# Kernel optimization log

Measured on AMD Instinct MI355X. Metric: run time of the kernel, lower is better.

The kernel has to match this reference:

```python
import jax, jax.numpy as jnp
import numpy as np

B, CIN, H, W = 4, 64, 160, 160
G, K = 8, 3
KK = K * K
PAD = K // 2
CG = CIN // G  # channels per deformable group


def setup_inputs() -> dict:
    key = jax.random.key(0)
    ks = jax.random.split(key, 6)
    x = jax.random.normal(ks[0], (B, CIN, H, W), jnp.float32)
    feat = jax.random.normal(ks[1], (B, CIN, H, W), jnp.float32)
    # conv_offset weights (zero-init in the original; small random here so offsets are nontrivial)
    w_off = jax.random.normal(ks[2], (3 * G * KK, CIN, 3, 3), jnp.float32) * 0.01
    b_off = jax.random.normal(ks[3], (3 * G * KK,), jnp.float32) * 0.01
    # deformable conv weights (torchvision DeformConv2d: groups=1, bias=True)
    w_dcn = jax.random.normal(ks[4], (CIN, CIN, K, K), jnp.float32) * (1.0 / np.sqrt(CIN * KK))
    b_dcn = jax.random.normal(ks[5], (CIN,), jnp.float32) * 0.01
    return dict(x=x, feat=feat, w_off=w_off, b_off=b_off, w_dcn=w_dcn, b_dcn=b_dcn)


def _modulated_deform_conv(x, offset, mask, w, b):
    # x: [B,C,H,W]; offset: [B,2*G*KK,H,W] (interleaved dy,dx per (g,k));
    # mask: [B,G*KK,H,W]; w: [Cout,C,K,K]; stride 1, zero padding K//2.
    Bn, C, Hh, Ww = x.shape
    off = offset.reshape(Bn, G, KK, 2, Hh, Ww)
    dy = off[:, :, :, 0]  # [B,G,KK,H,W]
    dx = off[:, :, :, 1]
    ki = jnp.arange(K)
    base_y = (jnp.repeat(ki, K) - PAD).reshape(1, 1, KK, 1, 1).astype(x.dtype)
    base_x = (jnp.tile(ki, K) - PAD).reshape(1, 1, KK, 1, 1).astype(x.dtype)
    hy = jnp.arange(Hh, dtype=x.dtype).reshape(1, 1, 1, Hh, 1)
    wx = jnp.arange(Ww, dtype=x.dtype).reshape(1, 1, 1, 1, Ww)
    py = hy + base_y + dy  # sample rows  [B,G,KK,H,W]
    px = wx + base_x + dx  # sample cols
    y0 = jnp.floor(py)
    x0 = jnp.floor(px)
    ly = py - y0
    lx = px - x0
    y0i = y0.astype(jnp.int32)
    x0i = x0.astype(jnp.int32)
    xg = x.reshape(Bn, G, CG, Hh * Ww)

    def gather(yi, xi):
        valid = ((yi >= 0) & (yi < Hh) & (xi >= 0) & (xi < Ww)).astype(x.dtype)
        idx = jnp.clip(yi, 0, Hh - 1) * Ww + jnp.clip(xi, 0, Ww - 1)
        flat = idx.reshape(Bn, G, 1, KK * Hh * Ww)
        v = jnp.take_along_axis(xg, flat, axis=3).reshape(Bn, G, CG, KK, Hh, Ww)
        return v * valid[:, :, None]  # zero padding outside

    v = ((1 - ly) * (1 - lx))[:, :, None] * gather(y0i, x0i) \
      + ((1 - ly) * lx)[:, :, None] * gather(y0i, x0i + 1) \
      + (ly * (1 - lx))[:, :, None] * gather(y0i + 1, x0i) \
      + (ly * lx)[:, :, None] * gather(y0i + 1, x0i + 1)
    v = v * mask.reshape(Bn, G, 1, KK, Hh, Ww)
    wr = w.reshape(w.shape[0], G, CG, KK)
    out = jnp.einsum('ogck,bgckhw->bohw', wr, v) + b[None, :, None, None]
    return out


def reference(x, feat, w_off, b_off, w_dcn, b_dcn):
    # conv_offset: 3x3 conv, stride 1, pad 1
    out = jax.lax.conv_general_dilated(
        feat, w_off, (1, 1), ((1, 1), (1, 1)),
        dimension_numbers=('NCHW', 'OIHW', 'NCHW')) + b_off[None, :, None, None]
    o1, o2, m = jnp.split(out, 3, axis=1)
    offset = jnp.concatenate([o1, o2], axis=1)  # [B, 2*G*KK, H, W]
    mask = jax.nn.sigmoid(m)                    # [B, G*KK, H, W]
    return _modulated_deform_conv(x, offset, mask, w_dcn, b_dcn)
```

## Files before the change

kernel.cpp:

```cpp
#include <hip/hip_runtime.h>
#include <math.h>

#define Bn   4
#define CINc 64
#define Hh   160
#define Ww   160
#define Gg   8
#define HW   (Hh * Ww)
#define COFF 216

#define OROW 220
#define VROW 200
#define OFFS_SZ (64 * OROW)
#define UNION_SZ 12800

typedef short bf16x8 __attribute__((ext_vector_type(8)));
typedef float f32x4  __attribute__((ext_vector_type(4)));

static __device__ __forceinline__ unsigned short f2bf(float f) {
    unsigned int u = __float_as_uint(f);
    u = (u + 0x7fffu + ((u >> 16) & 1u)) >> 16;
    return (unsigned short)u;
}
static __device__ __forceinline__ float bf2f(unsigned short s) {
    return __uint_as_float(((unsigned int)s) << 16);
}
static __device__ __forceinline__ float blo(unsigned int u) {
    return __uint_as_float(u << 16);
}
static __device__ __forceinline__ float bhi(unsigned int u) {
    return __uint_as_float(u & 0xffff0000u);
}

#define WB 180
__global__ __launch_bounds__(256)
void prep_kernel(const float* __restrict__ feat, const float* __restrict__ x,
                 const float* __restrict__ w_off, const float* __restrict__ w_dcn,
                 unsigned short* __restrict__ featT, unsigned short* __restrict__ xG,
                 unsigned short* __restrict__ wofrag, unsigned short* __restrict__ wfrag) {
    const int blk = blockIdx.x;
    const int t = threadIdx.x;
    if (blk < 1280) {
        __shared__ float tile[CINc][161];
        const int isx = blk >= 640;
        const int rem = isx ? blk - 640 : blk;
        const int b = rem / Hh;
        const int h = rem % Hh;
        const float* src = isx ? x : feat;
        for (int i = t; i < CINc * (Ww / 4); i += 256) {
            int ci = i / (Ww / 4), w4 = i % (Ww / 4);
            float4 v = *(const float4*)(src + (((size_t)b * CINc + ci) * Hh + h) * Ww + w4 * 4);
            tile[ci][w4 * 4 + 0] = v.x; tile[ci][w4 * 4 + 1] = v.y;
            tile[ci][w4 * 4 + 2] = v.z; tile[ci][w4 * 4 + 3] = v.w;
        }
        __syncthreads();
        if (isx) {
            for (int i = t; i < CINc * Ww / 2; i += 256) {
                int g = i / (Ww * 4);
                int r = i % (Ww * 4);
                int w = r >> 2, cp = r & 3;
                unsigned int lo = f2bf(tile[g * 8 + 2 * cp][w]);
                unsigned int hi = f2bf(tile[g * 8 + 2 * cp + 1][w]);
                *(unsigned int*)(xG + (((size_t)b * Gg + g) * HW + h * Ww + w) * 8 + 2 * cp)
                    = lo | (hi << 16);
            }
        } else {
            for (int i = t; i < CINc * Ww / 2; i += 256) {
                int w = i / (CINc / 2), cp = i % (CINc / 2);
                unsigned int lo = f2bf(tile[2 * cp][w]);
                unsigned int hi = f2bf(tile[2 * cp + 1][w]);
                *(unsigned int*)(featT + (((size_t)b * Hh + h) * Ww + w) * CINc + 2 * cp)
                    = lo | (hi << 16);
            }
        }
    } else {
        for (int e = (blk - 1280) * 256 + t; e < 147456 + 36864; e += WB * 256) {
            if (e < 147456) {
                const int j    = e & 7;
                const int lane = (e >> 3) & 63;
                const int rest = e >> 9;
                const int mt = rest & 15;
                const int q  = rest >> 4;
                const int ks = q & 1;
                const int kp = q >> 1;
                const int co = mt * 16 + (lane & 15);
                const int ci = ks * 32 + (lane >> 4) * 8 + j;
                float v = (co < COFF) ? w_off[(size_t)co * 576 + ci * 9 + kp] : 0.f;
                wofrag[e] = f2bf(v);
            } else {
                const int e2   = e - 147456;
                const int j    = e2 & 7;
                const int lane = (e2 >> 3) & 63;
                const int mt   = (e2 >> 9) & 3;
                const int ks   = e2 >> 11;
                const int m = mt * 16 + (lane & 15);
                const int k = ks * 32 + (lane >> 4) * 8 + j;
                const int g = k / 72, r = k % 72;
                const int kk = r >> 3, cg = r & 7;
                const int ci = g * 8 + cg;
                wfrag[e2] = f2bf(w_dcn[((size_t)m * CINc + ci) * 9 + kk]);
            }
        }
    }
}

#define BLEND_J(out_, w00, w01, w10, w11, c00, c01, c10, c11) {            \
    float vl_ = (c00) * blo(w00) + (c01) * blo(w01)                        \
              + (c10) * blo(w10) + (c11) * blo(w11);                       \
    float vh_ = (c00) * bhi(w00) + (c01) * bhi(w01)                        \
              + (c10) * bhi(w10) + (c11) * bhi(w11);                       \
    asm("v_cvt_pk_bf16_f32 %0, %1, %2" : "=v"(out_) : "v"(vl_), "v"(vh_)); \
}

__global__ __launch_bounds__(256, 3)
void dcnpack_fused(const unsigned short* __restrict__ featT,
                   const unsigned short* __restrict__ xG,
                   const unsigned short* __restrict__ wofrag,
                   const unsigned short* __restrict__ wfrag,
                   const float* __restrict__ b_off,
                   const float* __restrict__ b_dcn,
                   float* __restrict__ out) {
    __shared__ unsigned short smem[OFFS_SZ + UNION_SZ];
    unsigned short* offs = smem;
    unsigned short* halo = smem + OFFS_SZ;
    unsigned short* vbuf = smem + OFFS_SZ;

    const int b  = blockIdx.z;
    const int h0 = blockIdx.y * 8;
    const int w0 = blockIdx.x * 8;
    const int t  = threadIdx.x;
    const int wv   = t >> 6;
    const int lane = t & 63;
    const int n    = lane & 15;
    const int kg   = lane >> 4;

    for (int task = t; task < 800; task += 256) {
        const int pix = task >> 3, ch = task & 7;
        const int ry = pix / 10, rx = pix % 10;
        const int gh = h0 - 1 + ry, gw = w0 - 1 + rx;
        float4 v = make_float4(0.f, 0.f, 0.f, 0.f);
        if (gh >= 0 && gh < Hh && gw >= 0 && gw < Ww)
            v = *(const float4*)(featT + ((((size_t)b * Hh) + gh) * Ww + gw) * CINc + ch * 8);
        *(float4*)(halo + pix * 72 + ch * 8) = v;
    }
    __syncthreads();

    const int bbase0 = (((n >> 3) * 10) + (n & 7)) * 72 + kg * 8;

    f32x4 cacc[4][4] = {};
    bf16x8 af[3][4];
    #pragma unroll
    for (int i = 0; i < 4; ++i)
        af[0][i] = *(const bf16x8*)(wofrag + (((size_t)0 * 16 + wv + 4 * i) * 64 + lane) * 8);
    #pragma unroll
    for (int i = 0; i < 4; ++i)
        af[1][i] = *(const bf16x8*)(wofrag + (((size_t)1 * 16 + wv + 4 * i) * 64 + lane) * 8);

    #pragma unroll
    for (int s = 0; s < 18; ++s) {
        if (s + 2 < 18) {
            #pragma unroll
            for (int i = 0; i < 4; ++i)
                af[(s + 2) % 3][i] = *(const bf16x8*)(wofrag +
                    (((size_t)(s + 2) * 16 + wv + 4 * i) * 64 + lane) * 8);
        }
        const int kp = s >> 1, ks = s & 1;
        const int ky = kp / 3, kx = kp % 3;
        #pragma unroll
        for (int nt = 0; nt < 4; ++nt) {
            const bf16x8 bfr = *(const bf16x8*)(halo + bbase0 + nt * 1440 +
                                                (ky * 10 + kx) * 72 + ks * 32);
            #pragma unroll
            for (int i = 0; i < 4; ++i)
                cacc[i][nt] = __builtin_amdgcn_mfma_f32_16x16x32_bf16(af[s % 3][i], bfr, cacc[i][nt], 0, 0, 0);
        }
    }

    #pragma unroll
    for (int i = 0; i < 4; ++i) {
        const int mt = wv + 4 * i;
        #pragma unroll
        for (int r = 0; r < 4; ++r) {
            const int co = mt * 16 + kg * 4 + r;
            if (co < COFF) {
                const float bias = b_off[co];
                const int ismask = (co >= 144);
                const int gk = ismask ? (co - 144) : (co >> 1);
                const int type = ismask ? 2 : (co & 1);
                #pragma unroll
                for (int nt = 0; nt < 4; ++nt) {
                    const int p = nt * 16 + n;
                    float v = cacc[i][nt][r] + bias;
                    if (ismask) v = 1.f / (1.f + expf(-v));
                    offs[p * OROW + gk * 3 + type] = f2bf(v);
                }
            }
        }
    }
    __syncthreads();

    f32x4 dacc[4] = {};
    const int p_t = t & 63;
    const int h_s = h0 + (p_t >> 3);
    const int w_s = w0 + (p_t & 7);

    for (int c = 0; c < 3; ++c) {
        float cf[6][4];
        uint4 q[6][4];
        #pragma unroll
        for (int it = 0; it < 6; ++it) {
            const int u = c * 24 + wv + it * 4;
            const int g = u / 9;
            const int k = u % 9;

            const float dy   = bf2f(offs[p_t * OROW + u * 3 + 0]);
            const float dx   = bf2f(offs[p_t * OROW + u * 3 + 1]);
            const float mask = bf2f(offs[p_t * OROW + u * 3 + 2]);

            const float py  = (float)h_s + (float)(k / 3 - 1) + dy;
            const float pxx = (float)w_s + (float)(k % 3 - 1) + dx;
            const float y0f = floorf(py), x0f = floorf(pxx);
            const float ly = py - y0f, lx = pxx - x0f;
            const int y0 = (int)y0f, x0i = (int)x0f;
            const int y1 = y0 + 1,  x1  = x0i + 1;

            const float vy0 = (y0 >= 0 && y0 < Hh) ? 1.f : 0.f;
            const float vy1 = (y1 >= 0 && y1 < Hh) ? 1.f : 0.f;
            const float vx0 = (x0i >= 0 && x0i < Ww) ? 1.f : 0.f;
            const float vx1 = (x1 >= 0 && x1 < Ww) ? 1.f : 0.f;

            cf[it][0] = (1.f - ly) * (1.f - lx) * vy0 * vx0 * mask;
            cf[it][1] = (1.f - ly) * lx         * vy0 * vx1 * mask;
            cf[it][2] = ly         * (1.f - lx) * vy1 * vx0 * mask;
            cf[it][3] = ly         * lx         * vy1 * vx1 * mask;

            const int y0c = min(max(y0, 0), Hh - 1), y1c = min(max(y1, 0), Hh - 1);
            const int x0c = min(max(x0i, 0), Ww - 1), x1c = min(max(x1, 0), Ww - 1);

            const unsigned short* xb = xG + ((size_t)b * Gg + g) * HW * 8;
            q[it][0] = *(const uint4*)(xb + ((size_t)y0c * Ww + x0c) * 8);
            q[it][1] = *(const uint4*)(xb + ((size_t)y0c * Ww + x1c) * 8);
            q[it][2] = *(const uint4*)(xb + ((size_t)y1c * Ww + x0c) * 8);
            q[it][3] = *(const uint4*)(xb + ((size_t)y1c * Ww + x1c) * 8);
        }

        #pragma unroll
        for (int it = 0; it < 6; ++it) {
            unsigned int rr0, rr1, rr2, rr3;
            BLEND_J(rr0, q[it][0].x, q[it][1].x, q[it][2].x, q[it][3].x,
                    cf[it][0], cf[it][1], cf[it][2], cf[it][3]);
            BLEND_J(rr1, q[it][0].y, q[it][1].y, q[it][2].y, q[it][3].y,
                    cf[it][0], cf[it][1], cf[it][2], cf[it][3]);
            BLEND_J(rr2, q[it][0].z, q[it][1].z, q[it][2].z, q[it][3].z,
                    cf[it][0], cf[it][1], cf[it][2], cf[it][3]);
            BLEND_J(rr3, q[it][0].w, q[it][1].w, q[it][2].w, q[it][3].w,
                    cf[it][0], cf[it][1], cf[it][2], cf[it][3]);
            uint4 res; res.x = rr0; res.y = rr1; res.z = rr2; res.w = rr3;
            *(uint4*)(vbuf + (size_t)p_t * VROW + (wv + it * 4) * 8) = res;
        }

        bf16x8 afr[6];
        #pragma unroll
        for (int s = 0; s < 6; ++s)
            afr[s] = *(const bf16x8*)(wfrag + (((size_t)(c * 6 + s) * 4 + wv) * 64 + lane) * 8);

        __syncthreads();

        #pragma unroll
        for (int s = 0; s < 6; ++s) {
            #pragma unroll
            for (int nt = 0; nt < 4; ++nt) {
                const bf16x8 bfr = *(const bf16x8*)(vbuf + (nt * 16 + n) * VROW + s * 32 + kg * 8);
                dacc[nt] = __builtin_amdgcn_mfma_f32_16x16x32_bf16(afr[s], bfr, dacc[nt], 0, 0, 0);
            }
        }
        __syncthreads();
    }

    #pragma unroll
    for (int nt = 0; nt < 4; ++nt) {
        const int p = nt * 16 + n;
        const int h = h0 + (p >> 3);
        const int w = w0 + (p & 7);
        #pragma unroll
        for (int r = 0; r < 4; ++r) {
            const int o = wv * 16 + kg * 4 + r;
            out[(((size_t)b * CINc + o) * HW) + h * Ww + w] = dacc[nt][r] + b_dcn[o];
        }
    }
}

extern "C" void kernel_launch(void* const* d_in, const int* in_sizes, int n_in,
                              void* d_out, int out_size, void* d_ws, size_t ws_size,
                              hipStream_t stream) {
    const float* x     = (const float*)d_in[0];
    const float* feat  = (const float*)d_in[1];
    const float* w_off = (const float*)d_in[2];
    const float* b_off = (const float*)d_in[3];
    const float* w_dcn = (const float*)d_in[4];
    const float* b_dcn = (const float*)d_in[5];
    float* out = (float*)d_out;

    unsigned short* featT  = (unsigned short*)d_ws;
    unsigned short* xG     = featT + (size_t)Bn * HW * CINc;
    unsigned short* wofrag = xG + (size_t)Bn * HW * CINc;
    unsigned short* wfrag  = wofrag + (size_t)147456;

    prep_kernel<<<dim3(1280 + WB), 256, 0, stream>>>(
        feat, x, w_off, w_dcn, featT, xG, wofrag, wfrag);
    dcnpack_fused<<<dim3(Ww / 8, Hh / 8, Bn), 256, 0, stream>>>(
        featT, xG, wofrag, wfrag, b_off, b_dcn, out);
}
```

Baseline: 192.3 us.

## Split fused DCN kernel into offset-conv and sampling-GEMM kernels

Splits the single fused kernel into two. The first computes the offset/mask conv with MFMA and writes packed bf16 offsets and masks to workspace in a tile-major layout. The second reads them back, does the bilinear sampling and runs the DCN GEMM. Each kernel uses less shared memory and fewer registers, which allows higher occupancy (launch bounds 4 instead of 3). The cost is an extra launch and a global round-trip for the offsets and masks. The old fused path is kept as a fallback when the workspace is too small.

```diff
diff --git a/kernel.cpp b/kernel.cpp
--- a/kernel.cpp
+++ b/kernel.cpp
@@ -8,6 +8,7 @@
 #define Gg   8
 #define HW   (Hh * Ww)
 #define COFF 216
+#define NTILE 400
 
 #define OROW 220
 #define VROW 200
@@ -112,6 +113,213 @@
     asm("v_cvt_pk_bf16_f32 %0, %1, %2" : "=v"(out_) : "v"(vl_), "v"(vh_)); \
 }
 
+__global__ __launch_bounds__(256, 4)
+void conv_off_kernel(const unsigned short* __restrict__ featT,
+                     const unsigned short* __restrict__ wofrag,
+                     const float* __restrict__ b_off,
+                     unsigned int* __restrict__ offYX,
+                     unsigned short* __restrict__ maskG) {
+    __shared__ unsigned short halo[100 * 72];
+
+    const int b  = blockIdx.z;
+    const int h0 = blockIdx.y * 8;
+    const int w0 = blockIdx.x * 8;
+    const int tile = blockIdx.y * 20 + blockIdx.x;
+    const int t  = threadIdx.x;
+    const int wv   = t >> 6;
+    const int lane = t & 63;
+    const int n    = lane & 15;
+    const int kg   = lane >> 4;
+
+    for (int task = t; task < 800; task += 256) {
+        const int pix = task >> 3, ch = task & 7;
+        const int ry = pix / 10, rx = pix % 10;
+        const int gh = h0 - 1 + ry, gw = w0 - 1 + rx;
+        float4 v = make_float4(0.f, 0.f, 0.f, 0.f);
+        if (gh >= 0 && gh < Hh && gw >= 0 && gw < Ww)
+            v = *(const float4*)(featT + ((((size_t)b * Hh) + gh) * Ww + gw) * CINc + ch * 8);
+        *(float4*)(halo + pix * 72 + ch * 8) = v;
+    }
+    __syncthreads();
+
+    const int bbase0 = (((n >> 3) * 10) + (n & 7)) * 72 + kg * 8;
+
+    f32x4 cacc[4][4] = {};
+    bf16x8 af[3][4];
+    #pragma unroll
+    for (int i = 0; i < 4; ++i)
+        af[0][i] = *(const bf16x8*)(wofrag + (((size_t)0 * 16 + wv + 4 * i) * 64 + lane) * 8);
+    #pragma unroll
+    for (int i = 0; i < 4; ++i)
+        af[1][i] = *(const bf16x8*)(wofrag + (((size_t)1 * 16 + wv + 4 * i) * 64 + lane) * 8);
+
+    #pragma unroll
+    for (int s = 0; s < 18; ++s) {
+        if (s + 2 < 18) {
+            #pragma unroll
+            for (int i = 0; i < 4; ++i)
+                af[(s + 2) % 3][i] = *(const bf16x8*)(wofrag +
+                    (((size_t)(s + 2) * 16 + wv + 4 * i) * 64 + lane) * 8);
+        }
+        const int kp = s >> 1, ks = s & 1;
+        const int ky = kp / 3, kx = kp % 3;
+        #pragma unroll
+        for (int nt = 0; nt < 4; ++nt) {
+            const bf16x8 bfr = *(const bf16x8*)(halo + bbase0 + nt * 1440 +
+                                                (ky * 10 + kx) * 72 + ks * 32);
+            #pragma unroll
+            for (int i = 0; i < 4; ++i)
+                cacc[i][nt] = __builtin_amdgcn_mfma_f32_16x16x32_bf16(af[s % 3][i], bfr, cacc[i][nt], 0, 0, 0);
+        }
+    }
+
+    #pragma unroll
+    for (int i = 0; i < 4; ++i) {
+        const int mt = wv + 4 * i;
+        #pragma unroll
+        for (int nt = 0; nt < 4; ++nt) {
+            const int p = nt * 16 + n;
+            if (mt < 9) {
+                const int cob = mt * 16 + kg * 4;
+                const int gkA = cob >> 1;
+                const float v0 = cacc[i][nt][0] + b_off[cob + 0];
+                const float v1 = cacc[i][nt][1] + b_off[cob + 1];
+                const float v2 = cacc[i][nt][2] + b_off[cob + 2];
+                const float v3 = cacc[i][nt][3] + b_off[cob + 3];
+                unsigned int w01, w23;
+                asm("v_cvt_pk_bf16_f32 %0, %1, %2" : "=v"(w01) : "v"(v0), "v"(v1));
+                asm("v_cvt_pk_bf16_f32 %0, %1, %2" : "=v"(w23) : "v"(v2), "v"(v3));
+                offYX[(((size_t)b * 72 + gkA)     * NTILE + tile) * 64 + p] = w01;
+                offYX[(((size_t)b * 72 + gkA + 1) * NTILE + tile) * 64 + p] = w23;
+            } else {
+                #pragma unroll
+                for (int r = 0; r < 4; ++r) {
+                    const int co = mt * 16 + kg * 4 + r;
+                    if (co < COFF) {
+                        float v = cacc[i][nt][r] + b_off[co];
+                        v = 1.f / (1.f + expf(-v));
+                        maskG[(((size_t)b * 72 + (co - 144)) * NTILE + tile) * 64 + p] = f2bf(v);
+                    }
+                }
+            }
+        }
+    }
+}
+
+__global__ __launch_bounds__(256, 4)
+void dcn_sample_gemm(const unsigned int* __restrict__ offYX,
+                     const unsigned short* __restrict__ maskG,
+                     const unsigned short* __restrict__ xG,
+                     const unsigned short* __restrict__ wfrag,
+                     const float* __restrict__ b_dcn,
+                     float* __restrict__ out) {
+    __shared__ unsigned short vbuf[64 * VROW];
+
+    const int b  = blockIdx.z;
+    const int h0 = blockIdx.y * 8;
+    const int w0 = blockIdx.x * 8;
+    const int tile = blockIdx.y * 20 + blockIdx.x;
+    const int t  = threadIdx.x;
+    const int wv   = t >> 6;
+    const int lane = t & 63;
+    const int n    = lane & 15;
+    const int kg   = lane >> 4;
+    const int p_t = t & 63;
+    const int h_s = h0 + (p_t >> 3);
+    const int w_s = w0 + (p_t & 7);
+    const float fh = (float)h_s;
+    const float fw = (float)w_s;
+
+    f32x4 dacc[4] = {};
+
+    for (int c = 0; c < 3; ++c) {
+        float cf[6][4];
+        uint4 q[6][4];
+        #pragma unroll
+        for (int it = 0; it < 6; ++it) {
+            const int u = __builtin_amdgcn_readfirstlane(c * 24 + wv + it * 4);
+            const int g = u / 9;
+            const int k = u % 9;
+
+            const size_t uidx = (((size_t)b * 72 + u) * NTILE + tile) * 64 + p_t;
+            const unsigned int yx = offYX[uidx];
+            const float dy   = blo(yx);
+            const float dx   = bhi(yx);
+            const float mask = bf2f(maskG[uidx]);
+
+            const float py  = fh + (float)(k / 3 - 1) + dy;
+            const float pxx = fw + (float)(k % 3 - 1) + dx;
+            const float y0f = floorf(py), x0f = floorf(pxx);
+            const float ly = py - y0f, lx = pxx - x0f;
+            const int y0 = (int)y0f, x0i = (int)x0f;
+            const int y1 = y0 + 1,  x1  = x0i + 1;
+
+            const float vy0 = (y0 >= 0 && y0 < Hh) ? 1.f : 0.f;
+            const float vy1 = (y1 >= 0 && y1 < Hh) ? 1.f : 0.f;
+            const float vx0 = (x0i >= 0 && x0i < Ww) ? 1.f : 0.f;
+            const float vx1 = (x1 >= 0 && x1 < Ww) ? 1.f : 0.f;
+
+            cf[it][0] = (1.f - ly) * (1.f - lx) * vy0 * vx0 * mask;
+            cf[it][1] = (1.f - ly) * lx         * vy0 * vx1 * mask;
+            cf[it][2] = ly         * (1.f - lx) * vy1 * vx0 * mask;
+            cf[it][3] = ly         * lx         * vy1 * vx1 * mask;
+
+            const int y0c = min(max(y0, 0), Hh - 1), y1c = min(max(y1, 0), Hh - 1);
+            const int x0c = min(max(x0i, 0), Ww - 1), x1c = min(max(x1, 0), Ww - 1);
+
+            const unsigned short* xb = xG + ((size_t)b * Gg + g) * HW * 8;
+            q[it][0] = *(const uint4*)(xb + ((size_t)y0c * Ww + x0c) * 8);
+            q[it][1] = *(const uint4*)(xb + ((size_t)y0c * Ww + x1c) * 8);
+            q[it][2] = *(const uint4*)(xb + ((size_t)y1c * Ww + x0c) * 8);
+            q[it][3] = *(const uint4*)(xb + ((size_t)y1c * Ww + x1c) * 8);
+        }
+
+        #pragma unroll
+        for (int it = 0; it < 6; ++it) {
+            unsigned int rr0, rr1, rr2, rr3;
+            BLEND_J(rr0, q[it][0].x, q[it][1].x, q[it][2].x, q[it][3].x,
+                    cf[it][0], cf[it][1], cf[it][2], cf[it][3]);
+            BLEND_J(rr1, q[it][0].y, q[it][1].y, q[it][2].y, q[it][3].y,
+                    cf[it][0], cf[it][1], cf[it][2], cf[it][3]);
+            BLEND_J(rr2, q[it][0].z, q[it][1].z, q[it][2].z, q[it][3].z,
+                    cf[it][0], cf[it][1], cf[it][2], cf[it][3]);
+            BLEND_J(rr3, q[it][0].w, q[it][1].w, q[it][2].w, q[it][3].w,
+                    cf[it][0], cf[it][1], cf[it][2], cf[it][3]);
+            uint4 res; res.x = rr0; res.y = rr1; res.z = rr2; res.w = rr3;
+            *(uint4*)(vbuf + (size_t)p_t * VROW + (wv + it * 4) * 8) = res;
+        }
+
+        bf16x8 afr[6];
+        #pragma unroll
+        for (int s = 0; s < 6; ++s)
+            afr[s] = *(const bf16x8*)(wfrag + (((size_t)(c * 6 + s) * 4 + wv) * 64 + lane) * 8);
+
+        __syncthreads();
+
+        #pragma unroll
+        for (int s = 0; s < 6; ++s) {
+            #pragma unroll
+            for (int nt = 0; nt < 4; ++nt) {
+                const bf16x8 bfr = *(const bf16x8*)(vbuf + (nt * 16 + n) * VROW + s * 32 + kg * 8);
+                dacc[nt] = __builtin_amdgcn_mfma_f32_16x16x32_bf16(afr[s], bfr, dacc[nt], 0, 0, 0);
+            }
+        }
+        __syncthreads();
+    }
+
+    #pragma unroll
+    for (int nt = 0; nt < 4; ++nt) {
+        const int p = nt * 16 + n;
+        const int h = h0 + (p >> 3);
+        const int w = w0 + (p & 7);
+        #pragma unroll
+        for (int r = 0; r < 4; ++r) {
+            const int o = wv * 16 + kg * 4 + r;
+            out[(((size_t)b * CINc + o) * HW) + h * Ww + w] = dacc[nt][r] + b_dcn[o];
+        }
+    }
+}
+
 __global__ __launch_bounds__(256, 3)
 void dcnpack_fused(const unsigned short* __restrict__ featT,
                    const unsigned short* __restrict__ xG,
@@ -301,13 +509,34 @@
     const float* b_dcn = (const float*)d_in[5];
     float* out = (float*)d_out;
 
-    unsigned short* featT  = (unsigned short*)d_ws;
-    unsigned short* xG     = featT + (size_t)Bn * HW * CINc;
-    unsigned short* wofrag = xG + (size_t)Bn * HW * CINc;
-    unsigned short* wfrag  = wofrag + (size_t)147456;
-
-    prep_kernel<<<dim3(1280 + WB), 256, 0, stream>>>(
-        feat, x, w_off, w_dcn, featT, xG, wofrag, wfrag);
-    dcnpack_fused<<<dim3(Ww / 8, Hh / 8, Bn), 256, 0, stream>>>(
-        featT, xG, wofrag, wfrag, b_off, b_dcn, out);
-}
+    const size_t FEATT_E = (size_t)Bn * HW * CINc;
+    const size_t OFF_E   = (size_t)Bn * 72 * HW;
+
+    const size_t need = OFF_E * 4 + FEATT_E * 2 * 2 + 147456 * 2 + 36864 * 2 + OFF_E * 2;
+
+    if (ws_size >= need) {
+        unsigned int*   offYX  = (unsigned int*)d_ws;
+        unsigned short* featT  = (unsigned short*)(offYX + OFF_E);
+        unsigned short* xG     = featT + FEATT_E;
+        unsigned short* wofrag = xG + FEATT_E;
+        unsigned short* wfrag  = wofrag + (size_t)147456;
+        unsigned short* maskG  = wfrag + (size_t)36864;
+
+        prep_kernel<<<dim3(1280 + WB), 256, 0, stream>>>(
+            feat, x, w_off, w_dcn, featT, xG, wofrag, wfrag);
+        conv_off_kernel<<<dim3(Ww / 8, Hh / 8, Bn), 256, 0, stream>>>(
+            featT, wofrag, b_off, offYX, maskG);
+        dcn_sample_gemm<<<dim3(Ww / 8, Hh / 8, Bn), 256, 0, stream>>>(
+            offYX, maskG, xG, wfrag, b_dcn, out);
+    } else {
+        unsigned short* featT  = (unsigned short*)d_ws;
+        unsigned short* xG     = featT + FEATT_E;
+        unsigned short* wofrag = xG + FEATT_E;
+        unsigned short* wfrag  = wofrag + (size_t)147456;
+
+        prep_kernel<<<dim3(1280 + WB), 256, 0, stream>>>(
+            feat, x, w_off, w_dcn, featT, xG, wofrag, wfrag);
+        dcnpack_fused<<<dim3(Ww / 8, Hh / 8, Bn), 256, 0, stream>>>(
+            featT, xG, wofrag, wfrag, b_off, b_dcn, out);
+    }
+}
```

Result: slower. 213.8 us (+11.2%).
